# Kernel optimization log

Measured on AMD Instinct MI355X. Metric: run time of the kernel, lower is better.

Reference implementation:

```python
import jax, jax.numpy as jnp
import numpy as np

B, L, D, H, DH = 2, 2048, 768, 12, 3072
HD = D // H          # head dim = 64
EPS = 1e-6
SCALE = float(np.sqrt(HD))


def setup_inputs() -> dict:
    key = jax.random.key(0)
    ks = jax.random.split(key, 24)
    w = lambda k, shape: jax.random.normal(k, shape, jnp.float32) * 0.02
    # RoPE angles: [L, HD//2]
    inv_freq = 1.0 / (10000.0 ** (jnp.arange(HD // 2, dtype=jnp.float32) / (HD // 2)))
    ang = jnp.arange(L, dtype=jnp.float32)[:, None] * inv_freq[None, :]
    return {
        "x": jax.random.normal(ks[0], (B, L, D), jnp.float32),
        "c": jax.random.normal(ks[1], (B, D), jnp.float32),
        "freqs_cos": jnp.cos(ang),
        "freqs_sin": jnp.sin(ang),
        "W_q": w(ks[2], (D, D)), "W_k": w(ks[3], (D, D)),
        "W_v": w(ks[4], (D, D)), "W_o": w(ks[5], (D, D)),
        "cond_w1": w(ks[6], (D, DH)), "cond_b1": jnp.zeros((DH,), jnp.float32),
        "cond_w2": w(ks[7], (DH, D)), "cond_b2": jnp.zeros((D,), jnp.float32),
        "attn_norm_w": jnp.ones((D,), jnp.float32),
        "attn_alpha": w(ks[8], (D, D)), "attn_beta": w(ks[9], (D, D)),
        "attn_gamma": w(ks[10], (D, D)),
        "ffn_gate": w(ks[11], (D, DH)), "ffn_hidden": w(ks[12], (D, DH)),
        "ffn_out": w(ks[13], (DH, D)),
        "ffn_norm_w": jnp.ones((D,), jnp.float32),
        "ffn_beta": w(ks[14], (D, D)), "ffn_gamma": w(ks[15], (D, D)),
    }


def _rms_norm(x, w):
    return w * x * jax.lax.rsqrt(jnp.mean(x * x, axis=-1, keepdims=True) + EPS)


def _rope(x, cos, sin):
    # x: [b, n, l, hd]; complex pairs are consecutive (even, odd) lanes
    x0, x1 = x[..., 0::2], x[..., 1::2]
    c, s = cos[None, None], sin[None, None]          # [1,1,l,hd//2]
    r0 = x0 * c - x1 * s
    r1 = x0 * s + x1 * c
    return jnp.stack([r0, r1], axis=-1).reshape(x.shape)


def _attention(h, cos, sin, W_q, W_k, W_v, W_o):
    b, l, d = h.shape
    split = lambda y: y.reshape(b, l, H, HD).transpose(0, 2, 1, 3)  # b n l hd
    q = _rope(split(h @ W_q), cos, sin)
    k = _rope(split(h @ W_k), cos, sin)
    v = split(h @ W_v)
    scores = jnp.einsum("bnld,bnmd->bnlm", q, k) / SCALE
    attn = jax.nn.softmax(scores, axis=-1)
    o = jnp.einsum("bnlm,bnmd->bnld", attn, v)
    return o.transpose(0, 2, 1, 3).reshape(b, l, d) @ W_o


def reference(x, c, freqs_cos, freqs_sin, W_q, W_k, W_v, W_o,
              cond_w1, cond_b1, cond_w2, cond_b2,
              attn_norm_w, attn_alpha, attn_beta, attn_gamma,
              ffn_gate, ffn_hidden, ffn_out, ffn_norm_w, ffn_beta, ffn_gamma):
    # conditioning embedding
    c2 = jax.nn.silu(c @ cond_w1 + cond_b1) @ cond_w2 + cond_b2   # [b, d]
    mod = lambda W: (c2 @ W)[:, None]                              # [b, 1, d]
    # attention sub-block with AdaLN modulation + alpha gating
    h = _rms_norm(x, attn_norm_w) * mod(attn_gamma) + mod(attn_beta)
    x = x + _attention(h, freqs_cos, freqs_sin, W_q, W_k, W_v, W_o) * mod(attn_alpha)
    # SwiGLU FFN sub-block (original gates the residual by ffn_gamma, not alpha)
    h = _rms_norm(x, ffn_norm_w) * mod(ffn_gamma) + mod(ffn_beta)
    ff = (jax.nn.silu(h @ ffn_gate) * (h @ ffn_hidden)) @ ffn_out
    return x + ff * mod(ffn_gamma)
```

## Files before the change

kernel.cpp:

```cpp
#include <hip/hip_runtime.h>

typedef unsigned short u16;
typedef __attribute__((ext_vector_type(8))) short short8;
typedef __attribute__((ext_vector_type(4))) float f32x4;

#define L_SEQ 2048
#define NHEAD 12
#define KVB 128
#define QBLK 128

__device__ __forceinline__ u16 f2bf(float f) {
    union { float f; unsigned u; } x; x.f = f;
    unsigned r = x.u + 0x7fffu + ((x.u >> 16) & 1u);
    return (u16)(r >> 16);
}
__device__ __forceinline__ float bf2f(u16 u) {
    union { unsigned u; float f; } x; x.u = ((unsigned)u) << 16;
    return x.f;
}
__device__ __forceinline__ float silu_f(float x) { return x / (1.f + __expf(-x)); }

__device__ __forceinline__ void gload16(const u16* g, u16* l) {
    __builtin_amdgcn_global_load_lds(
        (const __attribute__((address_space(1))) void*)g,
        (__attribute__((address_space(3))) void*)l, 16, 0, 0);
}

__global__ __launch_bounds__(256) void transpose_all(
    const float* __restrict__ S0, const float* __restrict__ S1,
    const float* __restrict__ S2, const float* __restrict__ S3,
    const float* __restrict__ S4, const float* __restrict__ S5,
    const float* __restrict__ S6,
    u16* __restrict__ D0, u16* __restrict__ D1, u16* __restrict__ D2,
    u16* __restrict__ D3, u16* __restrict__ D4, u16* __restrict__ D5,
    u16* __restrict__ D6)
{
    int id = blockIdx.x;
    const float* W; u16* Wt; int K, N, local;
    if (id < 2304) {
        int sec = id / 576; local = id - sec * 576; K = 768; N = 768;
        W  = (sec == 0) ? S0 : (sec == 1) ? S1 : (sec == 2) ? S2 : S3;
        Wt = (sec == 0) ? D0 : (sec == 1) ? D1 : (sec == 2) ? D2 : D3;
    } else if (id < 6912) {
        int sec = (id - 2304) / 2304; local = (id - 2304) - sec * 2304; K = 768; N = 3072;
        W = sec ? S5 : S4; Wt = sec ? D5 : D4;
    } else {
        local = id - 6912; K = 3072; N = 768; W = S6; Wt = D6;
    }
    int nx = N >> 5;
    int n0 = (local % nx) * 32, k0 = (local / nx) * 32;
    __shared__ float t[32][33];
    int tx = threadIdx.x & 31, ty = threadIdx.x >> 5;
#pragma unroll
    for (int i = 0; i < 4; i++)
        t[ty + 8 * i][tx] = W[(size_t)(k0 + ty + 8 * i) * N + n0 + tx];
    __syncthreads();
#pragma unroll
    for (int i = 0; i < 4; i++)
        Wt[(size_t)(n0 + ty + 8 * i) * K + k0 + tx] = f2bf(t[tx][ty + 8 * i]);
}

__global__ __launch_bounds__(256) void cond_mlp1(
    const float* __restrict__ c, const float* __restrict__ w1, float* __restrict__ part)
{
    int j = blockIdx.x * 256 + threadIdx.x;
    int d0 = blockIdx.y * 96;
    float a0 = 0.f, a1 = 0.f;
    for (int d = d0; d < d0 + 96; ++d) {
        float w = w1[(size_t)d * 3072 + j];
        a0 += c[d] * w;
        a1 += c[768 + d] * w;
    }
    part[(size_t)(blockIdx.y * 2 + 0) * 3072 + j] = a0;
    part[(size_t)(blockIdx.y * 2 + 1) * 3072 + j] = a1;
}

__global__ __launch_bounds__(256) void cond_mlp2(
    const float* __restrict__ part, const float* __restrict__ b1,
    const float* __restrict__ w2, float* __restrict__ c2part)
{
    __shared__ float hid[2][384];
    const int tid = threadIdx.x;
    const int d0 = blockIdx.y * 384;
    for (int i = tid; i < 768; i += 256) {
        int b = i / 384, dd = i - b * 384;
        float s = b1[d0 + dd];
#pragma unroll
        for (int p = 0; p < 8; p++) s += part[(size_t)(p * 2 + b) * 3072 + d0 + dd];
        hid[b][dd] = silu_f(s);
    }
    __syncthreads();
    int jj = tid & 63, kc = tid >> 6;
    int j = blockIdx.x * 64 + jj;
    float a0 = 0.f, a1 = 0.f;
    for (int dd = kc * 96; dd < kc * 96 + 96; ++dd) {
        float w = w2[(size_t)(d0 + dd) * 768 + j];
        a0 += hid[0][dd] * w;
        a1 += hid[1][dd] * w;
    }
    __shared__ float r0[256], r1[256];
    r0[tid] = a0; r1[tid] = a1;
    __syncthreads();
    if (kc == 0) {
        a0 = r0[jj] + r0[64 + jj] + r0[128 + jj] + r0[192 + jj];
        a1 = r1[jj] + r1[64 + jj] + r1[128 + jj] + r1[192 + jj];
        c2part[(size_t)(blockIdx.y * 2 + 0) * 768 + j] = a0;
        c2part[(size_t)(blockIdx.y * 2 + 1) * 768 + j] = a1;
    }
}

__global__ __launch_bounds__(256) void mod_gemm(
    const float* __restrict__ c2part, const float* __restrict__ b2,
    const float* __restrict__ W0, const float* __restrict__ W1,
    const float* __restrict__ W2, const float* __restrict__ W3,
    const float* __restrict__ W4, float* __restrict__ out)
{
    __shared__ float c2s[2][768];
    const int tid = threadIdx.x;
    for (int i = tid; i < 1536; i += 256) {
        int b = i / 768, d = i - b * 768;
        float s = b2[d];
#pragma unroll
        for (int p = 0; p < 8; p++) s += c2part[(size_t)(p * 2 + b) * 768 + d];
        c2s[b][d] = s;
    }
    __syncthreads();
    int w = blockIdx.y;
    const float* W = (w == 0) ? W0 : (w == 1) ? W1 : (w == 2) ? W2 : (w == 3) ? W3 : W4;
    int jj = tid & 63, kc = tid >> 6;
    int j = blockIdx.x * 64 + jj;
    float a0 = 0.f, a1 = 0.f;
    for (int d = kc * 192; d < kc * 192 + 192; ++d) {
        float ww = W[(size_t)d * 768 + j];
        a0 += c2s[0][d] * ww;
        a1 += c2s[1][d] * ww;
    }
    __shared__ float r0[256], r1[256];
    r0[tid] = a0; r1[tid] = a1;
    __syncthreads();
    if (kc == 0) {
        a0 = r0[jj] + r0[64 + jj] + r0[128 + jj] + r0[192 + jj];
        a1 = r1[jj] + r1[64 + jj] + r1[128 + jj] + r1[192 + jj];
        out[(size_t)(w * 2 + 0) * 768 + j] = a0;
        out[(size_t)(w * 2 + 1) * 768 + j] = a1;
    }
}

template<int IN>
__global__ __launch_bounds__(256) void rmsnorm_mod(
    const void* __restrict__ xin, const float* __restrict__ nw,
    const float* __restrict__ gamma, const float* __restrict__ beta,
    u16* __restrict__ hout)
{
    int row = blockIdx.x;
    int b = row >> 11;
    int t = threadIdx.x;
    float v0, v1, v2;
    if (IN == 0) {
        const float* xr = (const float*)xin + (size_t)row * 768;
        v0 = xr[t]; v1 = xr[t + 256]; v2 = xr[t + 512];
    } else {
        const u16* xr = (const u16*)xin + (size_t)row * 768;
        v0 = bf2f(xr[t]); v1 = bf2f(xr[t + 256]); v2 = bf2f(xr[t + 512]);
    }
    float ss = v0 * v0 + v1 * v1 + v2 * v2;
#pragma unroll
    for (int m = 1; m < 64; m <<= 1) ss += __shfl_xor(ss, m);
    __shared__ float red[4];
    if ((t & 63) == 0) red[t >> 6] = ss;
    __syncthreads();
    float tot = red[0] + red[1] + red[2] + red[3];
    float rr = rsqrtf(tot * (1.f / 768.f) + 1e-6f);
    u16* ho = hout + (size_t)row * 768;
    const float* g = gamma + (size_t)b * 768;
    const float* be = beta + (size_t)b * 768;
#pragma unroll
    for (int i = 0; i < 3; i++) {
        int col = t + i * 256;
        float v = (i == 0) ? v0 : (i == 1) ? v1 : v2;
        ho[col] = f2bf(v * rr * nw[col] * g[col] + be[col]);
    }
}


__global__ __launch_bounds__(256) void gemm_qkv_rope(
    const u16* __restrict__ A, const u16* __restrict__ Bt,
    const float* __restrict__ fc, const float* __restrict__ fs,
    u16* __restrict__ qo, u16* __restrict__ ko, u16* __restrict__ vt,
    int M, int N, int K)
{
    const float QSCALE = 0.125f * 1.44269504f;
    __shared__ __align__(16) u16 As[2][128 * 64];
    __shared__ __align__(16) u16 Bs[2][128 * 64];
    const int tid = threadIdx.x;
    const int lane = tid & 63, wid = tid >> 6;
    const int lo = lane & 15, hi = lane >> 4;
    const int bm = blockIdx.x * 128, bn = blockIdx.y * 128;
    const int wrow = (wid >> 1) * 64, wcol = (wid & 1) * 64;

    f32x4 acc[4][4];
#pragma unroll
    for (int a = 0; a < 4; a++)
#pragma unroll
        for (int b = 0; b < 4; b++)
            acc[a][b] = (f32x4){0.f, 0.f, 0.f, 0.f};

    auto stage = [&](int buf, int k0) {
#pragma unroll
        for (int p = 0; p < 4; p++) {
            int ch = tid + p * 256;
            int r = ch >> 3, g = ch & 7;
            gload16(A + (size_t)(bm + r) * K + k0 + ((g ^ (r & 7)) * 8), &As[buf][ch * 8]);
        }
#pragma unroll
        for (int p = 0; p < 4; p++) {
            int ch = tid + p * 256;
            int r = ch >> 3, g = ch & 7;
            gload16(Bt + (size_t)(bn + r) * K + k0 + ((g ^ (r & 7)) * 8), &Bs[buf][ch * 8]);
        }
    };

    stage(0, 0);
    int cur = 0;
    const int NT = K >> 6;
    for (int t = 0; t < NT; t++) {
        __syncthreads();
        if (t + 1 < NT) stage(cur ^ 1, (t + 1) * 64);
        short8 af[4][2], bfr[4][2];
#pragma unroll
        for (int mi = 0; mi < 4; mi++) {
            int r = wrow + mi * 16 + lo;
#pragma unroll
            for (int h = 0; h < 2; h++)
                af[mi][h] = *(const short8*)(&As[cur][r * 64 + (((h * 4 + hi) ^ (r & 7)) * 8)]);
        }
#pragma unroll
        for (int nj = 0; nj < 4; nj++) {
            int r = wcol + nj * 16 + lo;
#pragma unroll
            for (int h = 0; h < 2; h++)
                bfr[nj][h] = *(const short8*)(&Bs[cur][r * 64 + (((h * 4 + hi) ^ (r & 7)) * 8)]);
        }
        __builtin_amdgcn_s_setprio(1);
#pragma unroll
        for (int mi = 0; mi < 4; mi++)
#pragma unroll
            for (int nj = 0; nj < 4; nj++) {
                acc[mi][nj] = __builtin_amdgcn_mfma_f32_16x16x32_bf16(af[mi][0], bfr[nj][0], acc[mi][nj], 0, 0, 0);
                acc[mi][nj] = __builtin_amdgcn_mfma_f32_16x16x32_bf16(af[mi][1], bfr[nj][1], acc[mi][nj], 0, 0, 0);
            }
        __builtin_amdgcn_s_setprio(0);
        cur ^= 1;
    }
    const int which = bn / 768;
    if (which == 2) {
#pragma unroll
        for (int mi = 0; mi < 4; mi++)
#pragma unroll
            for (int nj = 0; nj < 4; nj++) {
                int row0 = bm + wrow + mi * 16 + hi * 4;
                int col = bn + wcol + nj * 16 + lo;
                int within = col - 1536;
                int h = within >> 6, d = within & 63;
                int l0 = row0 & (L_SEQ - 1), b = row0 >> 11;
                unsigned w0, w1;
                asm("v_cvt_pk_bf16_f32 %0, %1, %2" : "=v"(w0) : "v"(acc[mi][nj][0]), "v"(acc[mi][nj][1]));
                asm("v_cvt_pk_bf16_f32 %0, %1, %2" : "=v"(w1) : "v"(acc[mi][nj][2]), "v"(acc[mi][nj][3]));
                uint2 pk2; pk2.x = w0; pk2.y = w1;
                *(uint2*)(vt + (((size_t)(b * NHEAD + h)) * 64 + d) * L_SEQ + l0) = pk2;
            }
    } else {
#pragma unroll
        for (int mi = 0; mi < 4; mi++)
#pragma unroll
            for (int nj = 0; nj < 4; nj++)
#pragma unroll
                for (int i = 0; i < 4; i++) {
                    int row = bm + wrow + mi * 16 + hi * 4 + i;
                    int col = bn + wcol + nj * 16 + lo;
                    float v = acc[mi][nj][i];
                    int within = col - which * 768;
                    int h = within >> 6, d = within & 63;
                    int l = row & (L_SEQ - 1), b = row >> 11;
                    int dp = d >> 1;
                    float cc = fc[l * 32 + dp], sn = fs[l * 32 + dp];
                    float pv = __shfl_xor(v, 1);
                    float r_;
                    if ((lo & 1) == 0) r_ = v * cc - pv * sn;
                    else               r_ = pv * sn + v * cc;
                    if (which == 0) r_ *= QSCALE;
                    u16* dst = (which == 0) ? qo : ko;
                    dst[(((size_t)(b * NHEAD + h)) * L_SEQ + l) * 64 + d] = f2bf(r_);
                }
    }
}

template<int MODE>
__global__ __launch_bounds__(256) void gemm_res64(
    const u16* __restrict__ A, const u16* __restrict__ Bt,
    void* __restrict__ outp, const void* __restrict__ X, const float* __restrict__ coef,
    int M, int N, int K)
{
    __shared__ __align__(16) u16 As[2][64 * 64];
    __shared__ __align__(16) u16 Bs[2][128 * 64];
    const int tid = threadIdx.x;
    const int lane = tid & 63, wid = tid >> 6;
    const int lo = lane & 15, hi = lane >> 4;
    const int bm = blockIdx.x * 64, bn = blockIdx.y * 128;
    const int wrow = (wid >> 1) * 32, wcol = (wid & 1) * 64;

    f32x4 acc[2][4];
#pragma unroll
    for (int a = 0; a < 2; a++)
#pragma unroll
        for (int b = 0; b < 4; b++)
            acc[a][b] = (f32x4){0.f, 0.f, 0.f, 0.f};

    auto stage = [&](int buf, int k0) {
#pragma unroll
        for (int p = 0; p < 2; p++) {
            int ch = tid + p * 256;
            int r = ch >> 3, g = ch & 7;
            gload16(A + (size_t)(bm + r) * K + k0 + ((g ^ (r & 7)) * 8), &As[buf][ch * 8]);
        }
#pragma unroll
        for (int p = 0; p < 4; p++) {
            int ch = tid + p * 256;
            int r = ch >> 3, g = ch & 7;
            gload16(Bt + (size_t)(bn + r) * K + k0 + ((g ^ (r & 7)) * 8), &Bs[buf][ch * 8]);
        }
    };

    stage(0, 0);
    int cur = 0;
    const int NT = K >> 6;
    for (int t = 0; t < NT; t++) {
        __syncthreads();
        if (t + 1 < NT) stage(cur ^ 1, (t + 1) * 64);
        short8 af[2][2], bfr[4][2];
#pragma unroll
        for (int mi = 0; mi < 2; mi++) {
            int r = wrow + mi * 16 + lo;
#pragma unroll
            for (int h = 0; h < 2; h++)
                af[mi][h] = *(const short8*)(&As[cur][r * 64 + (((h * 4 + hi) ^ (r & 7)) * 8)]);
        }
#pragma unroll
        for (int nj = 0; nj < 4; nj++) {
            int r = wcol + nj * 16 + lo;
#pragma unroll
            for (int h = 0; h < 2; h++)
                bfr[nj][h] = *(const short8*)(&Bs[cur][r * 64 + (((h * 4 + hi) ^ (r & 7)) * 8)]);
        }
        __builtin_amdgcn_s_setprio(1);
#pragma unroll
        for (int mi = 0; mi < 2; mi++)
#pragma unroll
            for (int nj = 0; nj < 4; nj++) {
                acc[mi][nj] = __builtin_amdgcn_mfma_f32_16x16x32_bf16(af[mi][0], bfr[nj][0], acc[mi][nj], 0, 0, 0);
                acc[mi][nj] = __builtin_amdgcn_mfma_f32_16x16x32_bf16(af[mi][1], bfr[nj][1], acc[mi][nj], 0, 0, 0);
            }
        __builtin_amdgcn_s_setprio(0);
        cur ^= 1;
    }
#pragma unroll
    for (int mi = 0; mi < 2; mi++)
#pragma unroll
        for (int nj = 0; nj < 4; nj++)
#pragma unroll
            for (int i = 0; i < 4; i++) {
                int row = bm + wrow + mi * 16 + hi * 4 + i;
                int col = bn + wcol + nj * 16 + lo;
                size_t idx = (size_t)row * N + col;
                int b = row >> 11;
                float base = (MODE == 0) ? ((const float*)X)[idx]
                                         : bf2f(((const u16*)X)[idx]);
                float v = base + acc[mi][nj][i] * coef[(size_t)b * N + col];
                if (MODE == 0) ((u16*)outp)[idx] = f2bf(v);
                else           ((float*)outp)[idx] = v;
            }
}

__global__ __launch_bounds__(256) void gemm_ffn1(
    const u16* __restrict__ A, const u16* __restrict__ Gt, const u16* __restrict__ Ht,
    u16* __restrict__ ff, int M, int N, int K)
{
    __shared__ __align__(16) u16 As[2][128 * 64];
    __shared__ __align__(16) u16 Gs[2][64 * 64];
    __shared__ __align__(16) u16 Hs[2][64 * 64];
    const int tid = threadIdx.x;
    const int lane = tid & 63, wid = tid >> 6;
    const int lo = lane & 15, hi = lane >> 4;
    const int bm = blockIdx.x * 128, bn = blockIdx.y * 64;
    const int wrow = (wid >> 1) * 64, wcol = (wid & 1) * 32;

    f32x4 ag[4][2], ah[4][2];
#pragma unroll
    for (int a = 0; a < 4; a++)
#pragma unroll
        for (int b = 0; b < 2; b++) {
            ag[a][b] = (f32x4){0.f, 0.f, 0.f, 0.f};
            ah[a][b] = (f32x4){0.f, 0.f, 0.f, 0.f};
        }

    auto stage = [&](int buf, int k0) {
#pragma unroll
        for (int p = 0; p < 4; p++) {
            int ch = tid + p * 256;
            int r = ch >> 3, g = ch & 7;
            gload16(A + (size_t)(bm + r) * K + k0 + ((g ^ (r & 7)) * 8), &As[buf][ch * 8]);
        }
#pragma unroll
        for (int p = 0; p < 2; p++) {
            int ch = tid + p * 256;
            int r = ch >> 3, g = ch & 7;
            gload16(Gt + (size_t)(bn + r) * K + k0 + ((g ^ (r & 7)) * 8), &Gs[buf][ch * 8]);
        }
#pragma unroll
        for (int p = 0; p < 2; p++) {
            int ch = tid + p * 256;
            int r = ch >> 3, g = ch & 7;
            gload16(Ht + (size_t)(bn + r) * K + k0 + ((g ^ (r & 7)) * 8), &Hs[buf][ch * 8]);
        }
    };

    stage(0, 0);
    int cur = 0;
    const int NT = K >> 6;
    for (int t = 0; t < NT; t++) {
        __syncthreads();
        if (t + 1 < NT) stage(cur ^ 1, (t + 1) * 64);
        short8 af[4][2], gf[2][2], hf[2][2];
#pragma unroll
        for (int mi = 0; mi < 4; mi++) {
            int r = wrow + mi * 16 + lo;
#pragma unroll
            for (int h = 0; h < 2; h++)
                af[mi][h] = *(const short8*)(&As[cur][r * 64 + (((h * 4 + hi) ^ (r & 7)) * 8)]);
        }
#pragma unroll
        for (int nj = 0; nj < 2; nj++) {
            int r = wcol + nj * 16 + lo;
#pragma unroll
            for (int h = 0; h < 2; h++) {
                gf[nj][h] = *(const short8*)(&Gs[cur][r * 64 + (((h * 4 + hi) ^ (r & 7)) * 8)]);
                hf[nj][h] = *(const short8*)(&Hs[cur][r * 64 + (((h * 4 + hi) ^ (r & 7)) * 8)]);
            }
        }
        __builtin_amdgcn_s_setprio(1);
#pragma unroll
        for (int mi = 0; mi < 4; mi++)
#pragma unroll
            for (int nj = 0; nj < 2; nj++) {
                ag[mi][nj] = __builtin_amdgcn_mfma_f32_16x16x32_bf16(af[mi][0], gf[nj][0], ag[mi][nj], 0, 0, 0);
                ag[mi][nj] = __builtin_amdgcn_mfma_f32_16x16x32_bf16(af[mi][1], gf[nj][1], ag[mi][nj], 0, 0, 0);
                ah[mi][nj] = __builtin_amdgcn_mfma_f32_16x16x32_bf16(af[mi][0], hf[nj][0], ah[mi][nj], 0, 0, 0);
                ah[mi][nj] = __builtin_amdgcn_mfma_f32_16x16x32_bf16(af[mi][1], hf[nj][1], ah[mi][nj], 0, 0, 0);
            }
        __builtin_amdgcn_s_setprio(0);
        cur ^= 1;
    }
#pragma unroll
    for (int mi = 0; mi < 4; mi++)
#pragma unroll
        for (int nj = 0; nj < 2; nj++)
#pragma unroll
            for (int i = 0; i < 4; i++) {
                int row = bm + wrow + mi * 16 + hi * 4 + i;
                int col = bn + wcol + nj * 16 + lo;
                ff[(size_t)row * N + col] = f2bf(silu_f(ag[mi][nj][i]) * ah[mi][nj][i]);
            }
}

__global__ __launch_bounds__(512) void attn_fwd(
    const u16* __restrict__ q, const u16* __restrict__ k, const u16* __restrict__ vt,
    u16* __restrict__ outp)
{
    __shared__ __align__(16) u16 Kb[KVB * 64];
    __shared__ __align__(16) u16 Vb[64 * KVB];
    __shared__ __align__(16) u16 Ps[8][16 * KVB];
    const int tid = threadIdx.x;
    const int lane = tid & 63, wid = tid >> 6;
    const int lo = lane & 15, hi = lane >> 4;
    const int lid = blockIdx.x;
    const int xcd = lid & 7, li = lid >> 3;
    const int bh = xcd * 3 + (li >> 4);
    const int qt = li & 15;
    const int b = bh / NHEAD, h = bh % NHEAD;
    const int q0 = qt * QBLK + wid * 16;
    const u16* qb = q + ((size_t)bh * L_SEQ + q0) * 64;
    const u16* kbase = k + (size_t)bh * L_SEQ * 64;
    const u16* vbase = vt + (size_t)bh * 64 * L_SEQ;

    short8 qa0 = *(const short8*)(qb + lo * 64 + hi * 8);
    short8 qa1 = *(const short8*)(qb + lo * 64 + 32 + hi * 8);

    f32x4 oacc[4];
#pragma unroll
    for (int dt = 0; dt < 4; dt++) oacc[dt] = (f32x4){0.f, 0.f, 0.f, 0.f};
    float m_ = -1e30f, ls = 0.f;

    const int rk = tid >> 3, gk = tid & 7;
    const u16* ka = kbase + (size_t)rk * 64 + ((gk ^ (rk & 7)) * 8);
    const int rv = tid >> 4, gv = tid & 15;
    const u16* va = vbase + (size_t)rv * L_SEQ + ((gv ^ (rv & 15)) * 8);
    u16* kdst = &Kb[tid * 8];
    u16* vdst = &Vb[tid * 8];

    int4 kr0, kr1, vr0, vr1;
    kr0 = *(const int4*)(ka);
    kr1 = *(const int4*)(ka + 4096);
    vr0 = *(const int4*)(va);
    vr1 = *(const int4*)(va + 65536);

    const int NT = L_SEQ / KVB;
    u16* pw = &Ps[wid][0];
    const int pkey = lo << 3;
    for (int t = 0; t < NT; t++) {
        __syncthreads();
        *(int4*)(kdst)        = kr0;
        *(int4*)(kdst + 4096) = kr1;
        *(int4*)(vdst)        = vr0;
        *(int4*)(vdst + 4096) = vr1;
        __syncthreads();
        if (t + 1 < NT) {
            int kv0 = (t + 1) * KVB;
            const u16* kan = ka + (size_t)kv0 * 64;
            const u16* van = va + kv0;
            kr0 = *(const int4*)(kan);
            kr1 = *(const int4*)(kan + 4096);
            vr0 = *(const int4*)(van);
            vr1 = *(const int4*)(van + 65536);
        }
        f32x4 s[8];
#pragma unroll
        for (int nt = 0; nt < 8; nt++) {
            int kr_ = nt * 16 + lo;
            const u16* kp = &Kb[kr_ * 64];
            int key = (kr_ & 7) << 3;
            short8 kf0 = *(const short8*)(kp + ((hi * 8) ^ key));
            short8 kf1 = *(const short8*)(kp + ((32 + hi * 8) ^ key));
            __builtin_amdgcn_s_setprio(1);
            f32x4 z = (f32x4){0.f, 0.f, 0.f, 0.f};
            z = __builtin_amdgcn_mfma_f32_16x16x32_bf16(kf0, qa0, z, 0, 0, 0);
            s[nt] = __builtin_amdgcn_mfma_f32_16x16x32_bf16(kf1, qa1, s[nt] = z, 0, 0, 0);
            __builtin_amdgcn_s_setprio(0);
        }
        float t0 = fmaxf(fmaxf(s[0][0], s[0][1]), fmaxf(s[0][2], s[0][3]));
        float t1 = fmaxf(fmaxf(s[1][0], s[1][1]), fmaxf(s[1][2], s[1][3]));
        float t2 = fmaxf(fmaxf(s[2][0], s[2][1]), fmaxf(s[2][2], s[2][3]));
        float t3 = fmaxf(fmaxf(s[3][0], s[3][1]), fmaxf(s[3][2], s[3][3]));
        float t4 = fmaxf(fmaxf(s[4][0], s[4][1]), fmaxf(s[4][2], s[4][3]));
        float t5 = fmaxf(fmaxf(s[5][0], s[5][1]), fmaxf(s[5][2], s[5][3]));
        float t6 = fmaxf(fmaxf(s[6][0], s[6][1]), fmaxf(s[6][2], s[6][3]));
        float t7 = fmaxf(fmaxf(s[7][0], s[7][1]), fmaxf(s[7][2], s[7][3]));
        float pmax = fmaxf(fmaxf(fmaxf(t0, t1), fmaxf(t2, t3)),
                           fmaxf(fmaxf(t4, t5), fmaxf(t6, t7)));
        pmax = fmaxf(pmax, __shfl_xor(pmax, 16));
        pmax = fmaxf(pmax, __shfl_xor(pmax, 32));
        if (!__all(pmax - m_ <= 8.f)) {
            float mn = fmaxf(m_, pmax);
            float al = exp2f(m_ - mn);
            m_ = mn;
            ls *= al;
#pragma unroll
            for (int dt = 0; dt < 4; dt++) oacc[dt] *= al;
        }
        float rsA = 0.f, rsB = 0.f, rsC = 0.f, rsD = 0.f;
#pragma unroll
        for (int nt = 0; nt < 8; nt++) {
            float p0 = exp2f(s[nt][0] - m_);
            float p1 = exp2f(s[nt][1] - m_);
            float p2 = exp2f(s[nt][2] - m_);
            float p3 = exp2f(s[nt][3] - m_);
            s[nt][0] = p0; s[nt][1] = p1; s[nt][2] = p2; s[nt][3] = p3;
            rsA += p0; rsB += p1; rsC += p2; rsD += p3;
        }
        ls += (rsA + rsB) + (rsC + rsD);
#pragma unroll
        for (int nt = 0; nt < 8; nt++) {
            unsigned w0, w1;
            asm("v_cvt_pk_bf16_f32 %0, %1, %2" : "=v"(w0) : "v"(s[nt][0]), "v"(s[nt][1]));
            asm("v_cvt_pk_bf16_f32 %0, %1, %2" : "=v"(w1) : "v"(s[nt][2]), "v"(s[nt][3]));
            uint2 pk2; pk2.x = w0; pk2.y = w1;
            *(uint2*)(pw + lo * KVB + ((nt * 16 + hi * 4) ^ pkey)) = pk2;
        }
        short8 pa0 = *(const short8*)(pw + lo * KVB + ((0 * 32 + hi * 8) ^ pkey));
        short8 pa1 = *(const short8*)(pw + lo * KVB + ((1 * 32 + hi * 8) ^ pkey));
        short8 pa2 = *(const short8*)(pw + lo * KVB + ((2 * 32 + hi * 8) ^ pkey));
        short8 pa3 = *(const short8*)(pw + lo * KVB + ((3 * 32 + hi * 8) ^ pkey));
#pragma unroll
        for (int dt = 0; dt < 4; dt++) {
            int vr_ = dt * 16 + lo;
            const u16* vp = &Vb[vr_ * KVB];
            int vkey = (vr_ & 15) << 3;
            short8 vf0 = *(const short8*)(vp + ((0 * 32 + hi * 8) ^ vkey));
            short8 vf1 = *(const short8*)(vp + ((1 * 32 + hi * 8) ^ vkey));
            short8 vf2 = *(const short8*)(vp + ((2 * 32 + hi * 8) ^ vkey));
            short8 vf3 = *(const short8*)(vp + ((3 * 32 + hi * 8) ^ vkey));
            __builtin_amdgcn_s_setprio(1);
            oacc[dt] = __builtin_amdgcn_mfma_f32_16x16x32_bf16(vf0, pa0, oacc[dt], 0, 0, 0);
            oacc[dt] = __builtin_amdgcn_mfma_f32_16x16x32_bf16(vf1, pa1, oacc[dt], 0, 0, 0);
            oacc[dt] = __builtin_amdgcn_mfma_f32_16x16x32_bf16(vf2, pa2, oacc[dt], 0, 0, 0);
            oacc[dt] = __builtin_amdgcn_mfma_f32_16x16x32_bf16(vf3, pa3, oacc[dt], 0, 0, 0);
            __builtin_amdgcn_s_setprio(0);
        }
    }
    ls += __shfl_xor(ls, 16);
    ls += __shfl_xor(ls, 32);
    float inv = 1.f / ls;
    int qrow = q0 + lo;
    u16* orow = outp + ((size_t)(b * L_SEQ + qrow)) * 768 + h * 64;
#pragma unroll
    for (int dt = 0; dt < 4; dt++) {
        unsigned w0, w1;
        float o0 = oacc[dt][0] * inv, o1 = oacc[dt][1] * inv;
        float o2 = oacc[dt][2] * inv, o3 = oacc[dt][3] * inv;
        asm("v_cvt_pk_bf16_f32 %0, %1, %2" : "=v"(w0) : "v"(o0), "v"(o1));
        asm("v_cvt_pk_bf16_f32 %0, %1, %2" : "=v"(w1) : "v"(o2), "v"(o3));
        uint2 pk2; pk2.x = w0; pk2.y = w1;
        *(uint2*)(orow + dt * 16 + hi * 4) = pk2;
    }
}

extern "C" void kernel_launch(void* const* d_in, const int* in_sizes, int n_in,
                              void* d_out, int out_size, void* d_ws, size_t ws_size,
                              hipStream_t stream)
{
    const float* x      = (const float*)d_in[0];
    const float* c      = (const float*)d_in[1];
    const float* fcos   = (const float*)d_in[2];
    const float* fsin   = (const float*)d_in[3];
    const float* Wq     = (const float*)d_in[4];
    const float* Wk     = (const float*)d_in[5];
    const float* Wv     = (const float*)d_in[6];
    const float* Wo     = (const float*)d_in[7];
    const float* cw1    = (const float*)d_in[8];
    const float* cb1    = (const float*)d_in[9];
    const float* cw2    = (const float*)d_in[10];
    const float* cb2    = (const float*)d_in[11];
    const float* anw    = (const float*)d_in[12];
    const float* Walpha = (const float*)d_in[13];
    const float* Wbeta  = (const float*)d_in[14];
    const float* Wgamma = (const float*)d_in[15];
    const float* Wgate  = (const float*)d_in[16];
    const float* Whid   = (const float*)d_in[17];
    const float* Wout   = (const float*)d_in[18];
    const float* fnw    = (const float*)d_in[19];
    const float* Wbetaf = (const float*)d_in[20];
    const float* Wgammaf= (const float*)d_in[21];

    const int M = 4096;
    char* ws = (char*)d_ws;
    size_t off = 0;
    auto alloc = [&](size_t bytes) -> char* {
        char* p = ws + off;
        off += (bytes + 255) & ~(size_t)255;
        return p;
    };
    u16* wq_t   = (u16*)alloc((size_t)768 * 768 * 2);
    u16* wk_t   = (u16*)alloc((size_t)768 * 768 * 2);
    u16* wv_t   = (u16*)alloc((size_t)768 * 768 * 2);
    u16* wo_t   = (u16*)alloc((size_t)768 * 768 * 2);
    u16* gate_t = (u16*)alloc((size_t)3072 * 768 * 2);
    u16* hid_t  = (u16*)alloc((size_t)3072 * 768 * 2);
    u16* out_t  = (u16*)alloc((size_t)768 * 3072 * 2);
    float* part1 = (float*)alloc((size_t)8 * 2 * 3072 * 4);
    float* part2 = (float*)alloc((size_t)8 * 2 * 768 * 4);
    float* mods = (float*)alloc(5 * 2 * 768 * 4);
    u16* hbuf   = (u16*)alloc((size_t)M * 768 * 2);
    u16* qrope  = (u16*)alloc((size_t)M * 768 * 2);
    u16* krope  = (u16*)alloc((size_t)M * 768 * 2);
    u16* vtb    = (u16*)alloc((size_t)M * 768 * 2);
    u16* attnh  = (u16*)alloc((size_t)M * 768 * 2);
    u16* ybuf   = (u16*)alloc((size_t)M * 768 * 2);
    u16* ffbuf  = (u16*)alloc((size_t)M * 3072 * 2);

    transpose_all<<<9216, 256, 0, stream>>>(
        Wq, Wk, Wv, Wo, Wgate, Whid, Wout,
        wq_t, wk_t, wv_t, wo_t, gate_t, hid_t, out_t);

    cond_mlp1<<<dim3(12, 8), 256, 0, stream>>>(c, cw1, part1);
    cond_mlp2<<<dim3(12, 8), 256, 0, stream>>>(part1, cb1, cw2, part2);
    mod_gemm<<<dim3(12, 5), 256, 0, stream>>>(
        part2, cb2, Wgamma, Wbeta, Walpha, Wgammaf, Wbetaf, mods);

    rmsnorm_mod<0><<<M, 256, 0, stream>>>(x, anw, mods + 0 * 1536, mods + 1 * 1536, hbuf);

    gemm_qkv_rope<<<dim3(32, 18), 256, 0, stream>>>(
        hbuf, wq_t, fcos, fsin, qrope, krope, vtb, M, 2304, 768);

    attn_fwd<<<dim3(384), 512, 0, stream>>>(qrope, krope, vtb, attnh);

    gemm_res64<0><<<dim3(64, 6), 256, 0, stream>>>(
        attnh, wo_t, ybuf, x, mods + 2 * 1536, M, 768, 768);

    rmsnorm_mod<1><<<M, 256, 0, stream>>>(ybuf, fnw, mods + 3 * 1536, mods + 4 * 1536, hbuf);

    gemm_ffn1<<<dim3(32, 48), 256, 0, stream>>>(
        hbuf, gate_t, hid_t, ffbuf, M, 3072, 768);

    gemm_res64<1><<<dim3(64, 6), 256, 0, stream>>>(
        ffbuf, out_t, d_out, ybuf, mods + 3 * 1536, M, 768, 3072);
}
```

Baseline: 245.3 us.

## Stage GEMM tiles through registers with BK=128 single LDS buffer

The three GEMM kernels (QKV+RoPE, residual, SwiGLU) stop using direct global-to-LDS loads with a double buffer at K-tile 64. They now prefetch the next 128-wide K tile into registers while computing, then write it to a single LDS buffer between two barriers, using a 16-way XOR swizzle. This halves the number of K iterations and barriers per tile and lets global load latency overlap the MFMA work. In exchange it adds register pressure from the 16 int4 prefetch registers and an extra barrier per iteration, and LDS use per block stays the same or grows (64 KB in the QKV kernel), which may lower occupancy.

```diff
diff --git a/kernel.cpp b/kernel.cpp
--- a/kernel.cpp
+++ b/kernel.cpp
@@ -190,8 +190,8 @@
     int M, int N, int K)
 {
     const float QSCALE = 0.125f * 1.44269504f;
-    __shared__ __align__(16) u16 As[2][128 * 64];
-    __shared__ __align__(16) u16 Bs[2][128 * 64];
+    __shared__ __align__(16) u16 As[128 * 128];
+    __shared__ __align__(16) u16 Bs[128 * 128];
     const int tid = threadIdx.x;
     const int lane = tid & 63, wid = tid >> 6;
     const int lo = lane & 15, hi = lane >> 4;
@@ -205,52 +205,69 @@
         for (int b = 0; b < 4; b++)
             acc[a][b] = (f32x4){0.f, 0.f, 0.f, 0.f};
 
-    auto stage = [&](int buf, int k0) {
-#pragma unroll
-        for (int p = 0; p < 4; p++) {
-            int ch = tid + p * 256;
-            int r = ch >> 3, g = ch & 7;
-            gload16(A + (size_t)(bm + r) * K + k0 + ((g ^ (r & 7)) * 8), &As[buf][ch * 8]);
-        }
-#pragma unroll
-        for (int p = 0; p < 4; p++) {
-            int ch = tid + p * 256;
-            int r = ch >> 3, g = ch & 7;
-            gload16(Bt + (size_t)(bn + r) * K + k0 + ((g ^ (r & 7)) * 8), &Bs[buf][ch * 8]);
-        }
-    };
-
-    stage(0, 0);
-    int cur = 0;
-    const int NT = K >> 6;
+    const int rS = tid >> 4, gS = tid & 15;
+    const size_t kstep = 16 * (size_t)K;
+    const u16* baseA = A + (size_t)(bm + rS) * K + ((gS ^ (rS & 15)) * 8);
+    const u16* baseB = Bt + (size_t)(bn + rS) * K + ((gS ^ (rS & 15)) * 8);
+    u16* dstA = &As[tid * 8];
+    u16* dstB = &Bs[tid * 8];
+
+    int4 a0,a1,a2,a3,a4,a5,a6,a7, b0,b1,b2,b3,b4,b5,b6,b7;
+    a0 = *(const int4*)(baseA);             a1 = *(const int4*)(baseA + kstep);
+    a2 = *(const int4*)(baseA + 2 * kstep); a3 = *(const int4*)(baseA + 3 * kstep);
+    a4 = *(const int4*)(baseA + 4 * kstep); a5 = *(const int4*)(baseA + 5 * kstep);
+    a6 = *(const int4*)(baseA + 6 * kstep); a7 = *(const int4*)(baseA + 7 * kstep);
+    b0 = *(const int4*)(baseB);             b1 = *(const int4*)(baseB + kstep);
+    b2 = *(const int4*)(baseB + 2 * kstep); b3 = *(const int4*)(baseB + 3 * kstep);
+    b4 = *(const int4*)(baseB + 4 * kstep); b5 = *(const int4*)(baseB + 5 * kstep);
+    b6 = *(const int4*)(baseB + 6 * kstep); b7 = *(const int4*)(baseB + 7 * kstep);
+
+    const int NT = K >> 7;
     for (int t = 0; t < NT; t++) {
         __syncthreads();
-        if (t + 1 < NT) stage(cur ^ 1, (t + 1) * 64);
-        short8 af[4][2], bfr[4][2];
-#pragma unroll
-        for (int mi = 0; mi < 4; mi++) {
-            int r = wrow + mi * 16 + lo;
-#pragma unroll
-            for (int h = 0; h < 2; h++)
-                af[mi][h] = *(const short8*)(&As[cur][r * 64 + (((h * 4 + hi) ^ (r & 7)) * 8)]);
-        }
-#pragma unroll
-        for (int nj = 0; nj < 4; nj++) {
-            int r = wcol + nj * 16 + lo;
-#pragma unroll
-            for (int h = 0; h < 2; h++)
-                bfr[nj][h] = *(const short8*)(&Bs[cur][r * 64 + (((h * 4 + hi) ^ (r & 7)) * 8)]);
-        }
-        __builtin_amdgcn_s_setprio(1);
-#pragma unroll
-        for (int mi = 0; mi < 4; mi++)
+        *(int4*)(dstA)         = a0; *(int4*)(dstA + 2048)  = a1;
+        *(int4*)(dstA + 4096)  = a2; *(int4*)(dstA + 6144)  = a3;
+        *(int4*)(dstA + 8192)  = a4; *(int4*)(dstA + 10240) = a5;
+        *(int4*)(dstA + 12288) = a6; *(int4*)(dstA + 14336) = a7;
+        *(int4*)(dstB)         = b0; *(int4*)(dstB + 2048)  = b1;
+        *(int4*)(dstB + 4096)  = b2; *(int4*)(dstB + 6144)  = b3;
+        *(int4*)(dstB + 8192)  = b4; *(int4*)(dstB + 10240) = b5;
+        *(int4*)(dstB + 12288) = b6; *(int4*)(dstB + 14336) = b7;
+        __syncthreads();
+        if (t + 1 < NT) {
+            int k0 = (t + 1) * 128;
+            const u16* pA = baseA + k0;
+            const u16* pB = baseB + k0;
+            a0 = *(const int4*)(pA);             a1 = *(const int4*)(pA + kstep);
+            a2 = *(const int4*)(pA + 2 * kstep); a3 = *(const int4*)(pA + 3 * kstep);
+            a4 = *(const int4*)(pA + 4 * kstep); a5 = *(const int4*)(pA + 5 * kstep);
+            a6 = *(const int4*)(pA + 6 * kstep); a7 = *(const int4*)(pA + 7 * kstep);
+            b0 = *(const int4*)(pB);             b1 = *(const int4*)(pB + kstep);
+            b2 = *(const int4*)(pB + 2 * kstep); b3 = *(const int4*)(pB + 3 * kstep);
+            b4 = *(const int4*)(pB + 4 * kstep); b5 = *(const int4*)(pB + 5 * kstep);
+            b6 = *(const int4*)(pB + 6 * kstep); b7 = *(const int4*)(pB + 7 * kstep);
+        }
+#pragma unroll
+        for (int kk = 0; kk < 4; kk++) {
+            short8 af[4], bfr[4];
+#pragma unroll
+            for (int mi = 0; mi < 4; mi++) {
+                int r = wrow + mi * 16 + lo;
+                af[mi] = *(const short8*)(&As[r * 128 + (((kk * 4 + hi) ^ (r & 15)) * 8)]);
+            }
 #pragma unroll
             for (int nj = 0; nj < 4; nj++) {
-                acc[mi][nj] = __builtin_amdgcn_mfma_f32_16x16x32_bf16(af[mi][0], bfr[nj][0], acc[mi][nj], 0, 0, 0);
-                acc[mi][nj] = __builtin_amdgcn_mfma_f32_16x16x32_bf16(af[mi][1], bfr[nj][1], acc[mi][nj], 0, 0, 0);
-            }
-        __builtin_amdgcn_s_setprio(0);
-        cur ^= 1;
+                int r = wcol + nj * 16 + lo;
+                bfr[nj] = *(const short8*)(&Bs[r * 128 + (((kk * 4 + hi) ^ (r & 15)) * 8)]);
+            }
+            __builtin_amdgcn_s_setprio(1);
+#pragma unroll
+            for (int mi = 0; mi < 4; mi++)
+#pragma unroll
+                for (int nj = 0; nj < 4; nj++)
+                    acc[mi][nj] = __builtin_amdgcn_mfma_f32_16x16x32_bf16(af[mi], bfr[nj], acc[mi][nj], 0, 0, 0);
+            __builtin_amdgcn_s_setprio(0);
+        }
     }
     const int which = bn / 768;
     if (which == 2) {
@@ -301,8 +318,8 @@
     void* __restrict__ outp, const void* __restrict__ X, const float* __restrict__ coef,
     int M, int N, int K)
 {
-    __shared__ __align__(16) u16 As[2][64 * 64];
-    __shared__ __align__(16) u16 Bs[2][128 * 64];
+    __shared__ __align__(16) u16 As[64 * 128];
+    __shared__ __align__(16) u16 Bs[128 * 128];
     const int tid = threadIdx.x;
     const int lane = tid & 63, wid = tid >> 6;
     const int lo = lane & 15, hi = lane >> 4;
@@ -316,52 +333,63 @@
         for (int b = 0; b < 4; b++)
             acc[a][b] = (f32x4){0.f, 0.f, 0.f, 0.f};
 
-    auto stage = [&](int buf, int k0) {
-#pragma unroll
-        for (int p = 0; p < 2; p++) {
-            int ch = tid + p * 256;
-            int r = ch >> 3, g = ch & 7;
-            gload16(A + (size_t)(bm + r) * K + k0 + ((g ^ (r & 7)) * 8), &As[buf][ch * 8]);
-        }
-#pragma unroll
-        for (int p = 0; p < 4; p++) {
-            int ch = tid + p * 256;
-            int r = ch >> 3, g = ch & 7;
-            gload16(Bt + (size_t)(bn + r) * K + k0 + ((g ^ (r & 7)) * 8), &Bs[buf][ch * 8]);
-        }
-    };
-
-    stage(0, 0);
-    int cur = 0;
-    const int NT = K >> 6;
+    const int rS = tid >> 4, gS = tid & 15;
+    const size_t kstep = 16 * (size_t)K;
+    const u16* baseA = A + (size_t)(bm + rS) * K + ((gS ^ (rS & 15)) * 8);
+    const u16* baseB = Bt + (size_t)(bn + rS) * K + ((gS ^ (rS & 15)) * 8);
+    u16* dstA = &As[tid * 8];
+    u16* dstB = &Bs[tid * 8];
+
+    int4 a0,a1,a2,a3, b0,b1,b2,b3,b4,b5,b6,b7;
+    a0 = *(const int4*)(baseA);             a1 = *(const int4*)(baseA + kstep);
+    a2 = *(const int4*)(baseA + 2 * kstep); a3 = *(const int4*)(baseA + 3 * kstep);
+    b0 = *(const int4*)(baseB);             b1 = *(const int4*)(baseB + kstep);
+    b2 = *(const int4*)(baseB + 2 * kstep); b3 = *(const int4*)(baseB + 3 * kstep);
+    b4 = *(const int4*)(baseB + 4 * kstep); b5 = *(const int4*)(baseB + 5 * kstep);
+    b6 = *(const int4*)(baseB + 6 * kstep); b7 = *(const int4*)(baseB + 7 * kstep);
+
+    const int NT = K >> 7;
     for (int t = 0; t < NT; t++) {
         __syncthreads();
-        if (t + 1 < NT) stage(cur ^ 1, (t + 1) * 64);
-        short8 af[2][2], bfr[4][2];
-#pragma unroll
-        for (int mi = 0; mi < 2; mi++) {
-            int r = wrow + mi * 16 + lo;
-#pragma unroll
-            for (int h = 0; h < 2; h++)
-                af[mi][h] = *(const short8*)(&As[cur][r * 64 + (((h * 4 + hi) ^ (r & 7)) * 8)]);
-        }
-#pragma unroll
-        for (int nj = 0; nj < 4; nj++) {
-            int r = wcol + nj * 16 + lo;
-#pragma unroll
-            for (int h = 0; h < 2; h++)
-                bfr[nj][h] = *(const short8*)(&Bs[cur][r * 64 + (((h * 4 + hi) ^ (r & 7)) * 8)]);
-        }
-        __builtin_amdgcn_s_setprio(1);
-#pragma unroll
-        for (int mi = 0; mi < 2; mi++)
+        *(int4*)(dstA)        = a0; *(int4*)(dstA + 2048) = a1;
+        *(int4*)(dstA + 4096) = a2; *(int4*)(dstA + 6144) = a3;
+        *(int4*)(dstB)         = b0; *(int4*)(dstB + 2048)  = b1;
+        *(int4*)(dstB + 4096)  = b2; *(int4*)(dstB + 6144)  = b3;
+        *(int4*)(dstB + 8192)  = b4; *(int4*)(dstB + 10240) = b5;
+        *(int4*)(dstB + 12288) = b6; *(int4*)(dstB + 14336) = b7;
+        __syncthreads();
+        if (t + 1 < NT) {
+            int k0 = (t + 1) * 128;
+            const u16* pA = baseA + k0;
+            const u16* pB = baseB + k0;
+            a0 = *(const int4*)(pA);             a1 = *(const int4*)(pA + kstep);
+            a2 = *(const int4*)(pA + 2 * kstep); a3 = *(const int4*)(pA + 3 * kstep);
+            b0 = *(const int4*)(pB);             b1 = *(const int4*)(pB + kstep);
+            b2 = *(const int4*)(pB + 2 * kstep); b3 = *(const int4*)(pB + 3 * kstep);
+            b4 = *(const int4*)(pB + 4 * kstep); b5 = *(const int4*)(pB + 5 * kstep);
+            b6 = *(const int4*)(pB + 6 * kstep); b7 = *(const int4*)(pB + 7 * kstep);
+        }
+#pragma unroll
+        for (int kk = 0; kk < 4; kk++) {
+            short8 af[2], bfr[4];
+#pragma unroll
+            for (int mi = 0; mi < 2; mi++) {
+                int r = wrow + mi * 16 + lo;
+                af[mi] = *(const short8*)(&As[r * 128 + (((kk * 4 + hi) ^ (r & 15)) * 8)]);
+            }
 #pragma unroll
             for (int nj = 0; nj < 4; nj++) {
-                acc[mi][nj] = __builtin_amdgcn_mfma_f32_16x16x32_bf16(af[mi][0], bfr[nj][0], acc[mi][nj], 0, 0, 0);
-                acc[mi][nj] = __builtin_amdgcn_mfma_f32_16x16x32_bf16(af[mi][1], bfr[nj][1], acc[mi][nj], 0, 0, 0);
-            }
-        __builtin_amdgcn_s_setprio(0);
-        cur ^= 1;
+                int r = wcol + nj * 16 + lo;
+                bfr[nj] = *(const short8*)(&Bs[r * 128 + (((kk * 4 + hi) ^ (r & 15)) * 8)]);
+            }
+            __builtin_amdgcn_s_setprio(1);
+#pragma unroll
+            for (int mi = 0; mi < 2; mi++)
+#pragma unroll
+                for (int nj = 0; nj < 4; nj++)
+                    acc[mi][nj] = __builtin_amdgcn_mfma_f32_16x16x32_bf16(af[mi], bfr[nj], acc[mi][nj], 0, 0, 0);
+            __builtin_amdgcn_s_setprio(0);
+        }
     }
 #pragma unroll
     for (int mi = 0; mi < 2; mi++)
@@ -385,9 +413,9 @@
     const u16* __restrict__ A, const u16* __restrict__ Gt, const u16* __restrict__ Ht,
     u16* __restrict__ ff, int M, int N, int K)
 {
-    __shared__ __align__(16) u16 As[2][128 * 64];
-    __shared__ __align__(16) u16 Gs[2][64 * 64];
-    __shared__ __align__(16) u16 Hs[2][64 * 64];
+    __shared__ __align__(16) u16 As[128 * 128];
+    __shared__ __align__(16) u16 Gs[64 * 128];
+    __shared__ __align__(16) u16 Hs[64 * 128];
     const int tid = threadIdx.x;
     const int lane = tid & 63, wid = tid >> 6;
     const int lo = lane & 15, hi = lane >> 4;
@@ -403,62 +431,75 @@
             ah[a][b] = (f32x4){0.f, 0.f, 0.f, 0.f};
         }
 
-    auto stage = [&](int buf, int k0) {
-#pragma unroll
-        for (int p = 0; p < 4; p++) {
-            int ch = tid + p * 256;
-            int r = ch >> 3, g = ch & 7;
-            gload16(A + (size_t)(bm + r) * K + k0 + ((g ^ (r & 7)) * 8), &As[buf][ch * 8]);
-        }
-#pragma unroll
-        for (int p = 0; p < 2; p++) {
-            int ch = tid + p * 256;
-            int r = ch >> 3, g = ch & 7;
-            gload16(Gt + (size_t)(bn + r) * K + k0 + ((g ^ (r & 7)) * 8), &Gs[buf][ch * 8]);
-        }
-#pragma unroll
-        for (int p = 0; p < 2; p++) {
-            int ch = tid + p * 256;
-            int r = ch >> 3, g = ch & 7;
-            gload16(Ht + (size_t)(bn + r) * K + k0 + ((g ^ (r & 7)) * 8), &Hs[buf][ch * 8]);
-        }
-    };
-
-    stage(0, 0);
-    int cur = 0;
-    const int NT = K >> 6;
+    const int rS = tid >> 4, gS = tid & 15;
+    const size_t kstep = 16 * (size_t)K;
+    const u16* baseA = A + (size_t)(bm + rS) * K + ((gS ^ (rS & 15)) * 8);
+    const u16* baseG = Gt + (size_t)(bn + rS) * K + ((gS ^ (rS & 15)) * 8);
+    const u16* baseH = Ht + (size_t)(bn + rS) * K + ((gS ^ (rS & 15)) * 8);
+    u16* dstA = &As[tid * 8];
+    u16* dstG = &Gs[tid * 8];
+    u16* dstH = &Hs[tid * 8];
+
+    int4 a0,a1,a2,a3,a4,a5,a6,a7, g0,g1,g2,g3, h0,h1,h2,h3;
+    a0 = *(const int4*)(baseA);             a1 = *(const int4*)(baseA + kstep);
+    a2 = *(const int4*)(baseA + 2 * kstep); a3 = *(const int4*)(baseA + 3 * kstep);
+    a4 = *(const int4*)(baseA + 4 * kstep); a5 = *(const int4*)(baseA + 5 * kstep);
+    a6 = *(const int4*)(baseA + 6 * kstep); a7 = *(const int4*)(baseA + 7 * kstep);
+    g0 = *(const int4*)(baseG);             g1 = *(const int4*)(baseG + kstep);
+    g2 = *(const int4*)(baseG + 2 * kstep); g3 = *(const int4*)(baseG + 3 * kstep);
+    h0 = *(const int4*)(baseH);             h1 = *(const int4*)(baseH + kstep);
+    h2 = *(const int4*)(baseH + 2 * kstep); h3 = *(const int4*)(baseH + 3 * kstep);
+
+    const int NT = K >> 7;
     for (int t = 0; t < NT; t++) {
         __syncthreads();
-        if (t + 1 < NT) stage(cur ^ 1, (t + 1) * 64);
-        short8 af[4][2], gf[2][2], hf[2][2];
-#pragma unroll
-        for (int mi = 0; mi < 4; mi++) {
-            int r = wrow + mi * 16 + lo;
-#pragma unroll
-            for (int h = 0; h < 2; h++)
-                af[mi][h] = *(const short8*)(&As[cur][r * 64 + (((h * 4 + hi) ^ (r & 7)) * 8)]);
-        }
-#pragma unroll
-        for (int nj = 0; nj < 2; nj++) {
-            int r = wcol + nj * 16 + lo;
-#pragma unroll
-            for (int h = 0; h < 2; h++) {
-                gf[nj][h] = *(const short8*)(&Gs[cur][r * 64 + (((h * 4 + hi) ^ (r & 7)) * 8)]);
-                hf[nj][h] = *(const short8*)(&Hs[cur][r * 64 + (((h * 4 + hi) ^ (r & 7)) * 8)]);
-            }
-        }
-        __builtin_amdgcn_s_setprio(1);
-#pragma unroll
-        for (int mi = 0; mi < 4; mi++)
+        *(int4*)(dstA)         = a0; *(int4*)(dstA + 2048)  = a1;
+        *(int4*)(dstA + 4096)  = a2; *(int4*)(dstA + 6144)  = a3;
+        *(int4*)(dstA + 8192)  = a4; *(int4*)(dstA + 10240) = a5;
+        *(int4*)(dstA + 12288) = a6; *(int4*)(dstA + 14336) = a7;
+        *(int4*)(dstG)        = g0; *(int4*)(dstG + 2048) = g1;
+        *(int4*)(dstG + 4096) = g2; *(int4*)(dstG + 6144) = g3;
+        *(int4*)(dstH)        = h0; *(int4*)(dstH + 2048) = h1;
+        *(int4*)(dstH + 4096) = h2; *(int4*)(dstH + 6144) = h3;
+        __syncthreads();
+        if (t + 1 < NT) {
+            int k0 = (t + 1) * 128;
+            const u16* pA = baseA + k0;
+            const u16* pG = baseG + k0;
+            const u16* pH = baseH + k0;
+            a0 = *(const int4*)(pA);             a1 = *(const int4*)(pA + kstep);
+            a2 = *(const int4*)(pA + 2 * kstep); a3 = *(const int4*)(pA + 3 * kstep);
+            a4 = *(const int4*)(pA + 4 * kstep); a5 = *(const int4*)(pA + 5 * kstep);
+            a6 = *(const int4*)(pA + 6 * kstep); a7 = *(const int4*)(pA + 7 * kstep);
+            g0 = *(const int4*)(pG);             g1 = *(const int4*)(pG + kstep);
+            g2 = *(const int4*)(pG + 2 * kstep); g3 = *(const int4*)(pG + 3 * kstep);
+            h0 = *(const int4*)(pH);             h1 = *(const int4*)(pH + kstep);
+            h2 = *(const int4*)(pH + 2 * kstep); h3 = *(const int4*)(pH + 3 * kstep);
+        }
+#pragma unroll
+        for (int kk = 0; kk < 4; kk++) {
+            short8 af[4], gf[2], hf[2];
+#pragma unroll
+            for (int mi = 0; mi < 4; mi++) {
+                int r = wrow + mi * 16 + lo;
+                af[mi] = *(const short8*)(&As[r * 128 + (((kk * 4 + hi) ^ (r & 15)) * 8)]);
+            }
 #pragma unroll
             for (int nj = 0; nj < 2; nj++) {
-                ag[mi][nj] = __builtin_amdgcn_mfma_f32_16x16x32_bf16(af[mi][0], gf[nj][0], ag[mi][nj], 0, 0, 0);
-                ag[mi][nj] = __builtin_amdgcn_mfma_f32_16x16x32_bf16(af[mi][1], gf[nj][1], ag[mi][nj], 0, 0, 0);
-                ah[mi][nj] = __builtin_amdgcn_mfma_f32_16x16x32_bf16(af[mi][0], hf[nj][0], ah[mi][nj], 0, 0, 0);
-                ah[mi][nj] = __builtin_amdgcn_mfma_f32_16x16x32_bf16(af[mi][1], hf[nj][1], ah[mi][nj], 0, 0, 0);
-            }
-        __builtin_amdgcn_s_setprio(0);
-        cur ^= 1;
+                int r = wcol + nj * 16 + lo;
+                gf[nj] = *(const short8*)(&Gs[r * 128 + (((kk * 4 + hi) ^ (r & 15)) * 8)]);
+                hf[nj] = *(const short8*)(&Hs[r * 128 + (((kk * 4 + hi) ^ (r & 15)) * 8)]);
+            }
+            __builtin_amdgcn_s_setprio(1);
+#pragma unroll
+            for (int mi = 0; mi < 4; mi++)
+#pragma unroll
+                for (int nj = 0; nj < 2; nj++) {
+                    ag[mi][nj] = __builtin_amdgcn_mfma_f32_16x16x32_bf16(af[mi], gf[nj], ag[mi][nj], 0, 0, 0);
+                    ah[mi][nj] = __builtin_amdgcn_mfma_f32_16x16x32_bf16(af[mi], hf[nj], ah[mi][nj], 0, 0, 0);
+                }
+            __builtin_amdgcn_s_setprio(0);
+        }
     }
 #pragma unroll
     for (int mi = 0; mi < 4; mi++)
```

After: 246.3 us. Within noise of the previous version (+0.4%).

## Fold cond_mlp1 into transpose launch and interleave softmax with PV MFMAs

Applied to the files above, without the earlier changes.

The first conditioning-MLP stage becomes 96 extra blocks of the weight-transpose kernel, which removes one kernel launch and lets the two run concurrently. In the attention kernel, the exp/pack/store of P is split into four chunks, and each chunk's PV MFMAs are issued right after it is written. This lets matrix work overlap the exp math of the next chunk instead of waiting for the whole 128-wide tile. The risk is that each LDS write-then-read of P sits closer to its use, and the compiler's scheduling and register pressure may change.

```diff
diff --git a/kernel.cpp b/kernel.cpp
--- a/kernel.cpp
+++ b/kernel.cpp
@@ -33,9 +33,26 @@
     const float* __restrict__ S6,
     u16* __restrict__ D0, u16* __restrict__ D1, u16* __restrict__ D2,
     u16* __restrict__ D3, u16* __restrict__ D4, u16* __restrict__ D5,
-    u16* __restrict__ D6)
+    u16* __restrict__ D6,
+    const float* __restrict__ c, const float* __restrict__ w1,
+    float* __restrict__ part)
 {
     int id = blockIdx.x;
+    if (id >= 9216) {
+        int cid = id - 9216;
+        int bx = cid % 12, by = cid / 12;
+        int j = bx * 256 + threadIdx.x;
+        int d0 = by * 96;
+        float a0 = 0.f, a1 = 0.f;
+        for (int d = d0; d < d0 + 96; ++d) {
+            float w = w1[(size_t)d * 3072 + j];
+            a0 += c[d] * w;
+            a1 += c[768 + d] * w;
+        }
+        part[(size_t)(by * 2 + 0) * 3072 + j] = a0;
+        part[(size_t)(by * 2 + 1) * 3072 + j] = a1;
+        return;
+    }
     const float* W; u16* Wt; int K, N, local;
     if (id < 2304) {
         int sec = id / 576; local = id - sec * 576; K = 768; N = 768;
@@ -58,21 +75,6 @@
 #pragma unroll
     for (int i = 0; i < 4; i++)
         Wt[(size_t)(n0 + ty + 8 * i) * K + k0 + tx] = f2bf(t[tx][ty + 8 * i]);
-}
-
-__global__ __launch_bounds__(256) void cond_mlp1(
-    const float* __restrict__ c, const float* __restrict__ w1, float* __restrict__ part)
-{
-    int j = blockIdx.x * 256 + threadIdx.x;
-    int d0 = blockIdx.y * 96;
-    float a0 = 0.f, a1 = 0.f;
-    for (int d = d0; d < d0 + 96; ++d) {
-        float w = w1[(size_t)d * 3072 + j];
-        a0 += c[d] * w;
-        a1 += c[768 + d] * w;
-    }
-    part[(size_t)(blockIdx.y * 2 + 0) * 3072 + j] = a0;
-    part[(size_t)(blockIdx.y * 2 + 1) * 3072 + j] = a1;
 }
 
 __global__ __launch_bounds__(256) void cond_mlp2(
@@ -568,43 +570,40 @@
         }
         float rsA = 0.f, rsB = 0.f, rsC = 0.f, rsD = 0.f;
 #pragma unroll
-        for (int nt = 0; nt < 8; nt++) {
-            float p0 = exp2f(s[nt][0] - m_);
-            float p1 = exp2f(s[nt][1] - m_);
-            float p2 = exp2f(s[nt][2] - m_);
-            float p3 = exp2f(s[nt][3] - m_);
-            s[nt][0] = p0; s[nt][1] = p1; s[nt][2] = p2; s[nt][3] = p3;
-            rsA += p0; rsB += p1; rsC += p2; rsD += p3;
+        for (int kk = 0; kk < 4; kk++) {
+            const int nt0 = 2 * kk, nt1 = 2 * kk + 1;
+            float p00 = exp2f(s[nt0][0] - m_);
+            float p01 = exp2f(s[nt0][1] - m_);
+            float p02 = exp2f(s[nt0][2] - m_);
+            float p03 = exp2f(s[nt0][3] - m_);
+            float p10 = exp2f(s[nt1][0] - m_);
+            float p11 = exp2f(s[nt1][1] - m_);
+            float p12 = exp2f(s[nt1][2] - m_);
+            float p13 = exp2f(s[nt1][3] - m_);
+            rsA += p00 + p10; rsB += p01 + p11;
+            rsC += p02 + p12; rsD += p03 + p13;
+            unsigned w0, w1, w2, w3;
+            asm("v_cvt_pk_bf16_f32 %0, %1, %2" : "=v"(w0) : "v"(p00), "v"(p01));
+            asm("v_cvt_pk_bf16_f32 %0, %1, %2" : "=v"(w1) : "v"(p02), "v"(p03));
+            asm("v_cvt_pk_bf16_f32 %0, %1, %2" : "=v"(w2) : "v"(p10), "v"(p11));
+            asm("v_cvt_pk_bf16_f32 %0, %1, %2" : "=v"(w3) : "v"(p12), "v"(p13));
+            uint2 pkA; pkA.x = w0; pkA.y = w1;
+            uint2 pkB; pkB.x = w2; pkB.y = w3;
+            *(uint2*)(pw + lo * KVB + ((nt0 * 16 + hi * 4) ^ pkey)) = pkA;
+            *(uint2*)(pw + lo * KVB + ((nt1 * 16 + hi * 4) ^ pkey)) = pkB;
+            short8 pa = *(const short8*)(pw + lo * KVB + ((kk * 32 + hi * 8) ^ pkey));
+            __builtin_amdgcn_s_setprio(1);
+#pragma unroll
+            for (int dt = 0; dt < 4; dt++) {
+                int vr_ = dt * 16 + lo;
+                const u16* vp = &Vb[vr_ * KVB];
+                int vkey = (vr_ & 15) << 3;
+                short8 vf = *(const short8*)(vp + ((kk * 32 + hi * 8) ^ vkey));
+                oacc[dt] = __builtin_amdgcn_mfma_f32_16x16x32_bf16(vf, pa, oacc[dt], 0, 0, 0);
+            }
+            __builtin_amdgcn_s_setprio(0);
         }
         ls += (rsA + rsB) + (rsC + rsD);
-#pragma unroll
-        for (int nt = 0; nt < 8; nt++) {
-            unsigned w0, w1;
-            asm("v_cvt_pk_bf16_f32 %0, %1, %2" : "=v"(w0) : "v"(s[nt][0]), "v"(s[nt][1]));
-            asm("v_cvt_pk_bf16_f32 %0, %1, %2" : "=v"(w1) : "v"(s[nt][2]), "v"(s[nt][3]));
-            uint2 pk2; pk2.x = w0; pk2.y = w1;
-            *(uint2*)(pw + lo * KVB + ((nt * 16 + hi * 4) ^ pkey)) = pk2;
-        }
-        short8 pa0 = *(const short8*)(pw + lo * KVB + ((0 * 32 + hi * 8) ^ pkey));
-        short8 pa1 = *(const short8*)(pw + lo * KVB + ((1 * 32 + hi * 8) ^ pkey));
-        short8 pa2 = *(const short8*)(pw + lo * KVB + ((2 * 32 + hi * 8) ^ pkey));
-        short8 pa3 = *(const short8*)(pw + lo * KVB + ((3 * 32 + hi * 8) ^ pkey));
-#pragma unroll
-        for (int dt = 0; dt < 4; dt++) {
-            int vr_ = dt * 16 + lo;
-            const u16* vp = &Vb[vr_ * KVB];
-            int vkey = (vr_ & 15) << 3;
-            short8 vf0 = *(const short8*)(vp + ((0 * 32 + hi * 8) ^ vkey));
-            short8 vf1 = *(const short8*)(vp + ((1 * 32 + hi * 8) ^ vkey));
-            short8 vf2 = *(const short8*)(vp + ((2 * 32 + hi * 8) ^ vkey));
-            short8 vf3 = *(const short8*)(vp + ((3 * 32 + hi * 8) ^ vkey));
-            __builtin_amdgcn_s_setprio(1);
-            oacc[dt] = __builtin_amdgcn_mfma_f32_16x16x32_bf16(vf0, pa0, oacc[dt], 0, 0, 0);
-            oacc[dt] = __builtin_amdgcn_mfma_f32_16x16x32_bf16(vf1, pa1, oacc[dt], 0, 0, 0);
-            oacc[dt] = __builtin_amdgcn_mfma_f32_16x16x32_bf16(vf2, pa2, oacc[dt], 0, 0, 0);
-            oacc[dt] = __builtin_amdgcn_mfma_f32_16x16x32_bf16(vf3, pa3, oacc[dt], 0, 0, 0);
-            __builtin_amdgcn_s_setprio(0);
-        }
     }
     ls += __shfl_xor(ls, 16);
     ls += __shfl_xor(ls, 32);
@@ -676,11 +675,11 @@
     u16* ybuf   = (u16*)alloc((size_t)M * 768 * 2);
     u16* ffbuf  = (u16*)alloc((size_t)M * 3072 * 2);
 
-    transpose_all<<<9216, 256, 0, stream>>>(
+    transpose_all<<<9312, 256, 0, stream>>>(
         Wq, Wk, Wv, Wo, Wgate, Whid, Wout,
-        wq_t, wk_t, wv_t, wo_t, gate_t, hid_t, out_t);
-
-    cond_mlp1<<<dim3(12, 8), 256, 0, stream>>>(c, cw1, part1);
+        wq_t, wk_t, wv_t, wo_t, gate_t, hid_t, out_t,
+        c, cw1, part1);
+
     cond_mlp2<<<dim3(12, 8), 256, 0, stream>>>(part1, cb1, cw2, part2);
     mod_gemm<<<dim3(12, 5), 256, 0, stream>>>(
         part2, cb2, Wgamma, Wbeta, Walpha, Wgammaf, Wbetaf, mods);
```

Result: slower. 262.1 us (+6.9%).
